# Performance work log

Hardware: AMD Instinct MI355X
Metric: run time of the kernel (lower is better)

## Reference

```python
import jax, jax.numpy as jnp
import numpy as np

B, S, HID, H = 4, 1024, 1024, 16
D = HID // H


def setup_inputs() -> dict:
    key = jax.random.key(0)
    ks = jax.random.split(key, 4)
    scale = 0.02
    return {
        "hidden_states": jax.random.normal(ks[0], (B, S, HID), dtype=jnp.float32),
        "attention_mask": jnp.ones((B, S), dtype=jnp.int32),
        "layer_head_mask": jnp.ones((H,), dtype=jnp.float32),
        "Wq": jax.random.normal(ks[1], (HID, HID), dtype=jnp.float32) * scale,
        "bq": jnp.zeros((HID,), dtype=jnp.float32),
        "Wk": jax.random.normal(ks[2], (HID, HID), dtype=jnp.float32) * scale,
        "bk": jnp.zeros((HID,), dtype=jnp.float32),
        "Wv": jax.random.normal(ks[3], (HID, HID), dtype=jnp.float32) * scale,
        "bv": jnp.zeros((HID,), dtype=jnp.float32),
    }


def reference(hidden_states, attention_mask, layer_head_mask, Wq, bq, Wk, bk, Wv, bv):
    b, s, _ = hidden_states.shape
    # QKV projections, split heads: [B,S,H,D]
    q = (hidden_states @ Wq + bq).reshape(b, s, H, D)
    k = (hidden_states @ Wk + bk).reshape(b, s, H, D)
    v = (hidden_states @ Wv + bv).reshape(b, s, H, D)

    # attention bias from padding mask: [B,1,1,S]
    mask = attention_mask[:, None, None, :]
    neg = jnp.finfo(jnp.float32).min
    bias = jnp.where(mask > 0, 0.0, neg).astype(jnp.float32)

    # dot_product_attention_weights: scale query by 1/sqrt(D)
    q = q / jnp.sqrt(jnp.asarray(D, dtype=q.dtype))
    scores = jnp.einsum("bqhd,bkhd->bhqk", q, k) + bias  # [B,H,S,S]
    attn_weights = jax.nn.softmax(scores, axis=-1)

    # per-head masking
    attn_weights = attn_weights * layer_head_mask[None, :, None, None]

    attn_output = jnp.einsum("bhqk,bkhd->bqhd", attn_weights, v)
    return attn_output.reshape(b, s, HID)
```

## Files before the change

### kernel.cpp

```cpp
#include <hip/hip_runtime.h>
#include <stdint.h>

typedef __bf16 bf16_t;
typedef bf16_t __attribute__((ext_vector_type(8))) bf16x8;
typedef float __attribute__((ext_vector_type(4))) f32x4;
typedef float __attribute__((ext_vector_type(16))) f32x16;
typedef unsigned u32;

#define BATCH 4
#define SEQ 1024
#define HIDD 1024
#define NH 16
#define DH 64

__device__ __forceinline__ unsigned short f2bf(float f) {
  unsigned u = __float_as_uint(f);
  u += 0x7fffu + ((u >> 16) & 1u);
  return (unsigned short)(u >> 16);
}

__device__ __forceinline__ f32x4 mfma16(bf16x8 a, bf16x8 b, f32x4 c) {
  return __builtin_amdgcn_mfma_f32_16x16x32_bf16(a, b, c, 0, 0, 0);
}
__device__ __forceinline__ f32x16 mfma32(bf16x8 a, bf16x8 b, f32x16 c) {
  return __builtin_amdgcn_mfma_f32_32x32x16_bf16(a, b, c, 0, 0, 0);
}

__device__ __forceinline__ void gload_lds16(const void* g, void* l) {
  __builtin_amdgcn_global_load_lds(
      (__attribute__((address_space(1))) void*)(uintptr_t)g,
      (__attribute__((address_space(3))) void*)l, 16, 0, 0);
}

__device__ __forceinline__ u32 cvtpk(float lo, float hi) {
  u32 r;
  asm("v_cvt_pk_bf16_f32 %0, %1, %2" : "=v"(r) : "v"(lo), "v"(hi));
  return r;
}
__device__ __forceinline__ void plswap(u32& a, u32& b) {
  asm("v_permlane32_swap_b32 %0, %1" : "+v"(a), "+v"(b));
}

__global__ void hs2bf(const float* __restrict__ x, unsigned short* __restrict__ y) {
  const int i = blockIdx.x * 256 + threadIdx.x;
  const float4 f = ((const float4*)x)[i];
  ushort4 o = make_ushort4(f2bf(f.x), f2bf(f.y), f2bf(f.z), f2bf(f.w));
  ((ushort4*)y)[i] = o;
}

__global__ __launch_bounds__(256) void wtrans(
    const float* __restrict__ Wq, const float* __restrict__ Wk,
    const float* __restrict__ Wv, unsigned short* __restrict__ Wt) {
  __shared__ unsigned short tile[64][72];
  const int z = blockIdx.z;
  const float* W = (z == 0) ? Wq : (z == 1) ? Wk : Wv;
  unsigned short* o = Wt + (size_t)z * (1024 * 1024);
  const int k0 = blockIdx.x * 64, n0 = blockIdx.y * 64;
  const int r = threadIdx.x >> 6, c = threadIdx.x & 63;
#pragma unroll
  for (int i = 0; i < 16; ++i) {
    const int row = i * 4 + r;
    tile[row][c] = f2bf(W[(size_t)(k0 + row) * 1024 + n0 + c]);
  }
  __syncthreads();
#pragma unroll
  for (int i = 0; i < 16; ++i) {
    const int row = i * 4 + r;
    o[(size_t)(n0 + row) * 1024 + k0 + c] = tile[c][row];
  }
}

__global__ __launch_bounds__(256) void qkv_gemm(
    const unsigned short* __restrict__ A,
    const unsigned short* __restrict__ Wt,
    const float* __restrict__ bq, const float* __restrict__ bk,
    const float* __restrict__ bv,
    unsigned short* __restrict__ Qb,
    unsigned short* __restrict__ Kpk,
    unsigned short* __restrict__ Vpk) {
  __shared__ alignas(16) unsigned short Alds[128 * 32];
  __shared__ alignas(16) unsigned short Blds[128 * 32];

  const int z = blockIdx.z;
  const unsigned short* Bt = Wt + (size_t)z * (1024 * 1024);
  const float* bias = (z == 0) ? bq : (z == 1) ? bk : bv;
  const float scale = (z == 0) ? 0.125f * 1.44269504089f : 1.0f;

  const int m0 = blockIdx.x * 128;
  const int n0 = blockIdx.y * 128;
  const int t = threadIdx.x;
  const int w = t >> 6, l = t & 63;
  const int lg = l >> 4, lc = l & 15;
  const int wr = w >> 1, wc = w & 1;

  f32x4 acc[4][4] = {};

  for (int kt = 0; kt < 1024; kt += 32) {
    __syncthreads();
#pragma unroll
    for (int i = 0; i < 2; ++i) {
      const int c = i * 256 + t;
      const int row = c >> 2;
      const int kp = (c & 3) * 8;
      gload_lds16(A + (size_t)(m0 + row) * 1024 + kt + kp,
                  (char*)Alds + i * 4096 + w * 1024);
      gload_lds16(Bt + (size_t)(n0 + row) * 1024 + kt + kp,
                  (char*)Blds + i * 4096 + w * 1024);
    }
    __syncthreads();

    bf16x8 af[4], bfr[4];
#pragma unroll
    for (int m = 0; m < 4; ++m)
      af[m] = *(const bf16x8*)(Alds + (wr * 64 + m * 16 + lc) * 32 + lg * 8);
#pragma unroll
    for (int n = 0; n < 4; ++n)
      bfr[n] = *(const bf16x8*)(Blds + (wc * 64 + n * 16 + lc) * 32 + lg * 8);
#pragma unroll
    for (int m = 0; m < 4; ++m)
#pragma unroll
      for (int n = 0; n < 4; ++n)
        acc[m][n] = mfma16(af[m], bfr[n], acc[m][n]);
  }

  if (z == 0) {
#pragma unroll
    for (int n = 0; n < 4; ++n) {
      const int col = n0 + wc * 64 + n * 16 + lc;
      const float bs = bias[col];
#pragma unroll
      for (int m = 0; m < 4; ++m)
#pragma unroll
        for (int r = 0; r < 4; ++r) {
          const int row = m0 + wr * 64 + m * 16 + lg * 4 + r;
          Qb[(size_t)row * 1024 + col] = f2bf((acc[m][n][r] + bs) * scale);
        }
    }
  } else if (z == 1) {
#pragma unroll
    for (int n = 0; n < 4; ++n) {
      const int col = n0 + wc * 64 + n * 16 + lc;
      const float bs = bias[col];
      const int h = col >> 6, s = (col >> 4) & 3, hi = (col >> 3) & 1, e = col & 7;
#pragma unroll
      for (int m = 0; m < 4; ++m)
#pragma unroll
        for (int r = 0; r < 4; ++r) {
          const int row = m0 + wr * 64 + m * 16 + lg * 4 + r;
          const int bh = (row >> 10) * 16 + h, tl = row & 1023;
          const int kb = tl >> 5, lo = tl & 31;
          Kpk[(size_t)(((bh * 32 + kb) * 4 + s) * 512) + (lo + hi * 32) * 8 + e] =
              f2bf(acc[m][n][r] + bs);
        }
    }
  } else {
#pragma unroll
    for (int n = 0; n < 4; ++n) {
      const int col = n0 + wc * 64 + n * 16 + lc;
      const float bs = bias[col];
      const int h = col >> 6, g = (col >> 5) & 1, lo = col & 31;
#pragma unroll
      for (int m = 0; m < 4; ++m)
#pragma unroll
        for (int r = 0; r < 4; ++r) {
          const int row = m0 + wr * 64 + m * 16 + lg * 4 + r;
          const int bh = (row >> 10) * 16 + h, tl = row & 1023;
          const int kt = tl >> 6, within = tl & 63;
          const int sv = within >> 4, hiv = (within >> 3) & 1, ev = within & 7;
          Vpk[(size_t)(((bh * 16 + kt) * 8 + g * 4 + sv) * 512) +
              (lo + hiv * 32) * 8 + ev] = f2bf(acc[m][n][r] + bs);
        }
    }
  }
}

__global__ __launch_bounds__(256, 2) void attn_kernel(
    const unsigned short* __restrict__ Qb,
    const unsigned short* __restrict__ Kpack,
    const unsigned short* __restrict__ Vpack,
    const int* __restrict__ amask,
    const float* __restrict__ lhm,
    float* __restrict__ out) {
  __shared__ alignas(16) char K_lds[3][8192];
  __shared__ alignas(16) char V_lds[3][8192];

  const int id = blockIdx.x;
  const int swzid = (id & 7) * 64 + (id >> 3);
  const int qt = swzid & 7;
  const int bh = swzid >> 3;
  const int b = bh >> 4, h = bh & 15;
  const int t = threadIdx.x;
  const int w = t >> 6, l = t & 63;
  const int lo = l & 31, hi = l >> 5;
  const int q0 = qt * 128 + w * 32;

  const unsigned short* KpT = Kpack + (size_t)bh * 65536;
  const unsigned short* VpT = Vpack + (size_t)bh * 65536;
  const int soff = w * 512 + l * 8;

  auto stage = [&](int tk, int buf) {
    const unsigned short* ks = KpT + tk * 4096 + soff;
    const unsigned short* vs = VpT + tk * 4096 + soff;
    gload_lds16(ks, &K_lds[buf][w * 1024]);
    gload_lds16(ks + 2048, &K_lds[buf][4096 + w * 1024]);
    gload_lds16(vs, &V_lds[buf][w * 1024]);
    gload_lds16(vs + 2048, &V_lds[buf][4096 + w * 1024]);
  };

  const unsigned short* qp = Qb + (size_t)(b * SEQ + q0 + lo) * HIDD + h * DH + hi * 8;
  bf16x8 qf[4];
#pragma unroll
  for (int s = 0; s < 4; ++s) qf[s] = *(const bf16x8*)(qp + s * 16);

  bool needmask;
  {
    int andv = 1;
#pragma unroll
    for (int tkk = 0; tkk < 16; ++tkk)
      andv &= (amask[b * SEQ + tkk * 64 + l] > 0) ? 1 : 0;
    needmask = (__ballot(andv != 0) != ~0ull);
  }

  stage(0, 0);
  stage(1, 1);
  asm volatile("s_waitcnt vmcnt(4)" ::: "memory");
  asm volatile("s_barrier" ::: "memory");

  f32x16 sg0 = {}, sg1 = {};
  {
    const char* kb = K_lds[0];
    bf16x8 kf0[4], kf1[4];
#pragma unroll
    for (int s = 0; s < 4; ++s) {
      kf0[s] = *(const bf16x8*)(kb + s * 1024 + l * 16);
      kf1[s] = *(const bf16x8*)(kb + 4096 + s * 1024 + l * 16);
    }
    __builtin_amdgcn_s_setprio(1);
#pragma unroll
    for (int s = 0; s < 4; ++s) {
      sg0 = mfma32(kf0[s], qf[s], sg0);
      sg1 = mfma32(kf1[s], qf[s], sg1);
    }
    __builtin_amdgcn_s_setprio(0);
  }

  float m_run = -INFINITY, l_run = 0.f;
  f32x16 acc0 = {}, acc1 = {};
  int c0 = 0, c1 = 1, c2 = 2;

  for (int tk = 0; tk < 16; ++tk) {
    asm volatile("s_barrier" ::: "memory");
    if (tk < 14) {
      stage(tk + 2, c2);
      asm volatile("s_waitcnt vmcnt(4)" ::: "memory");
    } else {
      asm volatile("s_waitcnt vmcnt(0)" ::: "memory");
    }

    const char* vb = V_lds[c0];
    bf16x8 vf0[4], vf1[4];
#pragma unroll
    for (int s = 0; s < 4; ++s) {
      vf0[s] = *(const bf16x8*)(vb + s * 1024 + l * 16);
      vf1[s] = *(const bf16x8*)(vb + 4096 + s * 1024 + l * 16);
    }
    bf16x8 nk0[4], nk1[4];
    if (tk < 15) {
      const char* kb = K_lds[c1];
#pragma unroll
      for (int s = 0; s < 4; ++s) {
        nk0[s] = *(const bf16x8*)(kb + s * 1024 + l * 16);
        nk1[s] = *(const bf16x8*)(kb + 4096 + s * 1024 + l * 16);
      }
    }

    float t0[8];
#pragma unroll
    for (int i = 0; i < 8; ++i)
      t0[i] = fmaxf(fmaxf(sg0[i], sg0[i + 8]), fmaxf(sg1[i], sg1[i + 8]));
    float t1 = fmaxf(fmaxf(fmaxf(t0[0], t0[1]), fmaxf(t0[2], t0[3])),
                     fmaxf(fmaxf(t0[4], t0[5]), fmaxf(t0[6], t0[7])));
    const float pmax = fmaxf(t1, __shfl_xor(t1, 32));

    if (!__all(pmax <= m_run + 8.f)) {
      const float mnew = fmaxf(m_run, pmax);
      const float sc = __builtin_amdgcn_exp2f(m_run - mnew);
      m_run = mnew;
      l_run *= sc;
#pragma unroll
      for (int g = 0; g < 16; ++g) {
        const int rowi = (g & 3) + 8 * (g >> 2) + 4 * hi;
        const float scr = __shfl(sc, rowi);
        acc0[g] *= scr;
        acc1[g] *= scr;
      }
    }

#pragma unroll
    for (int g = 0; g < 16; ++g) {
      sg0[g] = __builtin_amdgcn_exp2f(sg0[g] - m_run);
      sg1[g] = __builtin_amdgcn_exp2f(sg1[g] - m_run);
    }

    if (needmask) {
      const int mv = amask[b * SEQ + tk * 64 + l];
      const unsigned long long m64 = __ballot(mv > 0);
      if (m64 != ~0ull) {
#pragma unroll
        for (int g = 0; g < 16; ++g) {
          const int krow = (g & 3) + 8 * (g >> 2) + 4 * hi;
          if (!((m64 >> krow) & 1)) sg0[g] = 0.f;
          if (!((m64 >> (krow + 32)) & 1)) sg1[g] = 0.f;
        }
      }
    }

    float s0[8];
#pragma unroll
    for (int i = 0; i < 8; ++i)
      s0[i] = (sg0[i] + sg0[i + 8]) + (sg1[i] + sg1[i + 8]);
    float rs = ((s0[0] + s0[1]) + (s0[2] + s0[3])) +
               ((s0[4] + s0[5]) + (s0[6] + s0[7]));
    rs += __shfl_xor(rs, 32);
    l_run += rs;

    auto mk = [](float a0, float a1, float a2, float a3,
                 float a4, float a5, float a6, float a7) -> bf16x8 {
      u32 x = cvtpk(a0, a1), y = cvtpk(a2, a3);
      u32 a = cvtpk(a4, a5), b2 = cvtpk(a6, a7);
      plswap(x, a);
      plswap(y, b2);
      union { u32 u[4]; bf16x8 v; } fu;
      fu.u[0] = x; fu.u[1] = y; fu.u[2] = a; fu.u[3] = b2;
      return fu.v;
    };
    const bf16x8 pa0 = mk(sg0[0], sg0[1], sg0[2], sg0[3], sg0[4], sg0[5], sg0[6], sg0[7]);
    const bf16x8 pa1 = mk(sg0[8], sg0[9], sg0[10], sg0[11], sg0[12], sg0[13], sg0[14], sg0[15]);
    const bf16x8 pa2 = mk(sg1[0], sg1[1], sg1[2], sg1[3], sg1[4], sg1[5], sg1[6], sg1[7]);
    const bf16x8 pa3 = mk(sg1[8], sg1[9], sg1[10], sg1[11], sg1[12], sg1[13], sg1[14], sg1[15]);

    __builtin_amdgcn_s_setprio(1);
#pragma unroll
    for (int s = 0; s < 4; ++s) {
      const bf16x8 paf = (s == 0) ? pa0 : (s == 1) ? pa1 : (s == 2) ? pa2 : pa3;
      acc0 = mfma32(paf, vf0[s], acc0);
      acc1 = mfma32(paf, vf1[s], acc1);
    }
    __builtin_amdgcn_s_setprio(0);

    if (tk < 15) {
      f32x16 a = {}, b2 = {};
      __builtin_amdgcn_s_setprio(1);
#pragma unroll
      for (int s = 0; s < 4; ++s) {
        a = mfma32(nk0[s], qf[s], a);
        b2 = mfma32(nk1[s], qf[s], b2);
      }
      __builtin_amdgcn_s_setprio(0);
      sg0 = a;
      sg1 = b2;
    }

    const int tmp = c0; c0 = c1; c1 = c2; c2 = tmp;
  }

  const float hm = lhm[h];
  const float inv = hm / l_run;
  float* ob = out + (size_t)(b * SEQ + q0) * HIDD + h * DH + lo;
#pragma unroll
  for (int g = 0; g < 16; ++g) {
    const int rowi = (g & 3) + 8 * (g >> 2) + 4 * hi;
    const float iv = __shfl(inv, rowi);
    ob[(size_t)rowi * HIDD] = acc0[g] * iv;
    ob[(size_t)rowi * HIDD + 32] = acc1[g] * iv;
  }
}

extern "C" void kernel_launch(void* const* d_in, const int* in_sizes, int n_in,
                              void* d_out, int out_size, void* d_ws, size_t ws_size,
                              hipStream_t stream) {
  const float* hs = (const float*)d_in[0];
  const int* amask = (const int*)d_in[1];
  const float* lhm = (const float*)d_in[2];
  const float* Wq = (const float*)d_in[3];
  const float* bq = (const float*)d_in[4];
  const float* Wk = (const float*)d_in[5];
  const float* bk = (const float*)d_in[6];
  const float* Wv = (const float*)d_in[7];
  const float* bv = (const float*)d_in[8];
  float* out = (float*)d_out;

  char* ws = (char*)d_ws;
  unsigned short* HSbf = (unsigned short*)ws;
  unsigned short* Wt = (unsigned short*)(ws + (8u << 20));
  unsigned short* Qb = (unsigned short*)(ws + (14u << 20));
  unsigned short* Kpk = (unsigned short*)(ws + (22u << 20));
  unsigned short* Vpk = (unsigned short*)(ws + (30u << 20));

  hs2bf<<<4096, 256, 0, stream>>>(hs, HSbf);
  wtrans<<<dim3(16, 16, 3), 256, 0, stream>>>(Wq, Wk, Wv, Wt);
  qkv_gemm<<<dim3(32, 8, 3), 256, 0, stream>>>(HSbf, Wt, bq, bk, bv, Qb, Kpk, Vpk);
  attn_kernel<<<512, 256, 0, stream>>>(Qb, Kpk, Vpk, amask, lhm, out);
}
```

Measured before the change: 88.52 us.

## Double-buffer QKV GEMM LDS tiles with BK=64 and MFMA-fragment layout

Rewrites the QKV projection GEMM main loop to use double-buffered LDS with a K-step of 64. The next tile's global-to-LDS loads are issued before computing on the current one, with explicit vmcnt waits and raw barriers. LDS is laid out directly in per-lane MFMA fragment order, so reads are contiguous 16-byte loads, and MFMA issue priority is raised. This is meant to hide global load latency and halve barrier count, at the cost of more LDS per block (64KB), which may reduce occupancy.

```diff
diff --git a/kernel.cpp b/kernel.cpp
--- a/kernel.cpp
+++ b/kernel.cpp
@@ -78,8 +78,8 @@
     unsigned short* __restrict__ Qb,
     unsigned short* __restrict__ Kpk,
     unsigned short* __restrict__ Vpk) {
-  __shared__ alignas(16) unsigned short Alds[128 * 32];
-  __shared__ alignas(16) unsigned short Blds[128 * 32];
+  __shared__ alignas(16) char A_lds[2][16384];
+  __shared__ alignas(16) char B_lds[2][16384];
 
   const int z = blockIdx.z;
   const unsigned short* Bt = Wt + (size_t)z * (1024 * 1024);
@@ -93,34 +93,55 @@
   const int lg = l >> 4, lc = l & 15;
   const int wr = w >> 1, wc = w & 1;
 
+  auto stage = [&](int kt, int buf) {
+#pragma unroll
+    for (int i = 0; i < 4; ++i) {
+      const int c = w + i * 4;
+      const int m = c & 7, ks = c >> 3;
+      const unsigned short* as =
+          A + (size_t)(m0 + m * 16 + lc) * 1024 + kt + ks * 32 + lg * 8;
+      const unsigned short* bs =
+          Bt + (size_t)(n0 + m * 16 + lc) * 1024 + kt + ks * 32 + lg * 8;
+      gload_lds16(as, &A_lds[buf][c * 1024]);
+      gload_lds16(bs, &B_lds[buf][c * 1024]);
+    }
+  };
+
   f32x4 acc[4][4] = {};
 
-  for (int kt = 0; kt < 1024; kt += 32) {
-    __syncthreads();
-#pragma unroll
-    for (int i = 0; i < 2; ++i) {
-      const int c = i * 256 + t;
-      const int row = c >> 2;
-      const int kp = (c & 3) * 8;
-      gload_lds16(A + (size_t)(m0 + row) * 1024 + kt + kp,
-                  (char*)Alds + i * 4096 + w * 1024);
-      gload_lds16(Bt + (size_t)(n0 + row) * 1024 + kt + kp,
-                  (char*)Blds + i * 4096 + w * 1024);
-    }
-    __syncthreads();
-
-    bf16x8 af[4], bfr[4];
-#pragma unroll
-    for (int m = 0; m < 4; ++m)
-      af[m] = *(const bf16x8*)(Alds + (wr * 64 + m * 16 + lc) * 32 + lg * 8);
-#pragma unroll
-    for (int n = 0; n < 4; ++n)
-      bfr[n] = *(const bf16x8*)(Blds + (wc * 64 + n * 16 + lc) * 32 + lg * 8);
-#pragma unroll
-    for (int m = 0; m < 4; ++m)
+  stage(0, 0);
+
+  for (int tkt = 0; tkt < 16; ++tkt) {
+    const int cur = tkt & 1;
+    if (tkt < 15) {
+      stage(tkt * 64 + 64, cur ^ 1);
+      asm volatile("s_waitcnt vmcnt(8)" ::: "memory");
+    } else {
+      asm volatile("s_waitcnt vmcnt(0)" ::: "memory");
+    }
+    __builtin_amdgcn_s_barrier();
+
+    const char* ab = A_lds[cur];
+    const char* bb = B_lds[cur];
+#pragma unroll
+    for (int ks = 0; ks < 2; ++ks) {
+      bf16x8 bfv[4];
 #pragma unroll
       for (int n = 0; n < 4; ++n)
-        acc[m][n] = mfma16(af[m], bfr[n], acc[m][n]);
+        bfv[n] = *(const bf16x8*)(bb + (ks * 8 + wc * 4 + n) * 1024 + l * 16);
+#pragma unroll
+      for (int m = 0; m < 4; ++m) {
+        const bf16x8 af =
+            *(const bf16x8*)(ab + (ks * 8 + wr * 4 + m) * 1024 + l * 16);
+        __builtin_amdgcn_s_setprio(1);
+#pragma unroll
+        for (int n = 0; n < 4; ++n)
+          acc[m][n] = mfma16(af, bfv[n], acc[m][n]);
+        __builtin_amdgcn_s_setprio(0);
+      }
+    }
+
+    __builtin_amdgcn_s_barrier();
   }
 
   if (z == 0) {
```

Result: slower. 106.2 us (+20.0%).

## Double-buffer LDS tiles in QKV GEMM and merge prep kernels into one launch

Applied to the files above, without the earlier changes.

The QKV projection GEMM now uses two LDS buffers per operand. The next K-tile is fetched with global-to-LDS loads while MFMAs run on the current tile, and there is one barrier per iteration instead of two. The hidden-state bf16 conversion and the weight transpose are merged into a single prep kernel that branches on block index, which removes one launch. The cost is twice the LDS footprint, and the compiler may insert conservative vmcnt waits around the LDS-DMA loads that limit the intended overlap.

```diff
diff --git a/kernel.cpp b/kernel.cpp
--- a/kernel.cpp
+++ b/kernel.cpp
@@ -41,21 +41,24 @@
   asm("v_permlane32_swap_b32 %0, %1" : "+v"(a), "+v"(b));
 }
 
-__global__ void hs2bf(const float* __restrict__ x, unsigned short* __restrict__ y) {
-  const int i = blockIdx.x * 256 + threadIdx.x;
-  const float4 f = ((const float4*)x)[i];
-  ushort4 o = make_ushort4(f2bf(f.x), f2bf(f.y), f2bf(f.z), f2bf(f.w));
-  ((ushort4*)y)[i] = o;
-}
-
-__global__ __launch_bounds__(256) void wtrans(
+__global__ __launch_bounds__(256) void prep(
+    const float* __restrict__ hs, unsigned short* __restrict__ HSbf,
     const float* __restrict__ Wq, const float* __restrict__ Wk,
     const float* __restrict__ Wv, unsigned short* __restrict__ Wt) {
   __shared__ unsigned short tile[64][72];
-  const int z = blockIdx.z;
+  const int bid = blockIdx.x;
+  if (bid < 4096) {
+    const int i = bid * 256 + threadIdx.x;
+    const float4 f = ((const float4*)hs)[i];
+    ushort4 o = make_ushort4(f2bf(f.x), f2bf(f.y), f2bf(f.z), f2bf(f.w));
+    ((ushort4*)HSbf)[i] = o;
+    return;
+  }
+  const int id = bid - 4096;
+  const int z = id >> 8, rem = id & 255;
+  const int k0 = (rem & 15) * 64, n0 = (rem >> 4) * 64;
   const float* W = (z == 0) ? Wq : (z == 1) ? Wk : Wv;
   unsigned short* o = Wt + (size_t)z * (1024 * 1024);
-  const int k0 = blockIdx.x * 64, n0 = blockIdx.y * 64;
   const int r = threadIdx.x >> 6, c = threadIdx.x & 63;
 #pragma unroll
   for (int i = 0; i < 16; ++i) {
@@ -78,8 +81,8 @@
     unsigned short* __restrict__ Qb,
     unsigned short* __restrict__ Kpk,
     unsigned short* __restrict__ Vpk) {
-  __shared__ alignas(16) unsigned short Alds[128 * 32];
-  __shared__ alignas(16) unsigned short Blds[128 * 32];
+  __shared__ alignas(16) unsigned short Alds[2][128 * 32];
+  __shared__ alignas(16) unsigned short Blds[2][128 * 32];
 
   const int z = blockIdx.z;
   const unsigned short* Bt = Wt + (size_t)z * (1024 * 1024);
@@ -93,29 +96,35 @@
   const int lg = l >> 4, lc = l & 15;
   const int wr = w >> 1, wc = w & 1;
 
-  f32x4 acc[4][4] = {};
-
-  for (int kt = 0; kt < 1024; kt += 32) {
-    __syncthreads();
+  auto stage = [&](int kt, int buf) {
 #pragma unroll
     for (int i = 0; i < 2; ++i) {
       const int c = i * 256 + t;
       const int row = c >> 2;
       const int kp = (c & 3) * 8;
       gload_lds16(A + (size_t)(m0 + row) * 1024 + kt + kp,
-                  (char*)Alds + i * 4096 + w * 1024);
+                  (char*)&Alds[buf][0] + i * 4096 + w * 1024);
       gload_lds16(Bt + (size_t)(n0 + row) * 1024 + kt + kp,
-                  (char*)Blds + i * 4096 + w * 1024);
-    }
+                  (char*)&Blds[buf][0] + i * 4096 + w * 1024);
+    }
+  };
+
+  f32x4 acc[4][4] = {};
+
+  stage(0, 0);
+
+  for (int tkt = 0; tkt < 32; ++tkt) {
+    const int cur = tkt & 1;
     __syncthreads();
+    if (tkt < 31) stage(tkt * 32 + 32, cur ^ 1);
 
     bf16x8 af[4], bfr[4];
 #pragma unroll
     for (int m = 0; m < 4; ++m)
-      af[m] = *(const bf16x8*)(Alds + (wr * 64 + m * 16 + lc) * 32 + lg * 8);
+      af[m] = *(const bf16x8*)(&Alds[cur][0] + (wr * 64 + m * 16 + lc) * 32 + lg * 8);
 #pragma unroll
     for (int n = 0; n < 4; ++n)
-      bfr[n] = *(const bf16x8*)(Blds + (wc * 64 + n * 16 + lc) * 32 + lg * 8);
+      bfr[n] = *(const bf16x8*)(&Blds[cur][0] + (wc * 64 + n * 16 + lc) * 32 + lg * 8);
 #pragma unroll
     for (int m = 0; m < 4; ++m)
 #pragma unroll
@@ -397,8 +406,7 @@
   unsigned short* Kpk = (unsigned short*)(ws + (22u << 20));
   unsigned short* Vpk = (unsigned short*)(ws + (30u << 20));
 
-  hs2bf<<<4096, 256, 0, stream>>>(hs, HSbf);
-  wtrans<<<dim3(16, 16, 3), 256, 0, stream>>>(Wq, Wk, Wv, Wt);
+  prep<<<4864, 256, 0, stream>>>(hs, HSbf, Wq, Wk, Wv, Wt);
   qkv_gemm<<<dim3(32, 8, 3), 256, 0, stream>>>(HSbf, Wt, bq, bk, bv, Qb, Kpk, Vpk);
   attn_kernel<<<512, 256, 0, stream>>>(Qb, Kpk, Vpk, amask, lhm, out);
 }
```

Measured after the change: 93.94 us. 6.1% more time.
